# Optimization experiments

Hardware: AMD Instinct MI355X
Metric: run time of the kernel (lower is better)

## Reference

```python
import jax, jax.numpy as jnp
import numpy as np

EMBED = 1024
HEADS = 16
HEAD_DIM = EMBED // HEADS


def setup_inputs() -> dict:
    key = jax.random.key(0)
    ks = jax.random.split(key, 7)
    N, S = 2, 2048
    k = jax.random.normal(ks[0], (N, S, EMBED), dtype=jnp.float32)
    q = jax.random.normal(ks[1], (N, S, EMBED), dtype=jnp.float32)
    v = jax.random.normal(ks[2], (N, S, EMBED), dtype=jnp.float32)
    sc = 1.0 / np.sqrt(HEAD_DIM)
    # nn.Linear weights, applied as x @ W.T
    Wk = jax.random.normal(ks[3], (HEAD_DIM, HEAD_DIM), dtype=jnp.float32) * sc
    Wq = jax.random.normal(ks[4], (HEAD_DIM, HEAD_DIM), dtype=jnp.float32) * sc
    Wv = jax.random.normal(ks[5], (HEAD_DIM, HEAD_DIM), dtype=jnp.float32) * sc
    Wo = jax.random.normal(ks[6], (EMBED, EMBED), dtype=jnp.float32) / np.sqrt(EMBED)
    return {"k": k, "q": q, "v": v, "Wk": Wk, "Wq": Wq, "Wv": Wv, "Wo": Wo}


def reference(k, q, v, Wk, Wq, Wv, Wo):
    N, S, _ = q.shape
    # reshape to [N, S, H, D]; per-head projection weights shared across heads
    kh = jnp.einsum('nshd,ed->nshe', k.reshape(N, S, HEADS, HEAD_DIM), Wk)
    qh = jnp.einsum('nshd,ed->nshe', q.reshape(N, S, HEADS, HEAD_DIM), Wq)
    vh = jnp.einsum('nshd,ed->nshe', v.reshape(N, S, HEADS, HEAD_DIM), Wv)
    # energy: [N, H, q_len, k_len]
    energy = jnp.einsum('nqhd,nkhd->nhqk', qh, kh)
    attn = jax.nn.softmax(energy / jnp.sqrt(jnp.float32(HEAD_DIM)), axis=-1)
    out = jnp.einsum('nhqk,nkhd->nqhd', attn, vh).reshape(N, S, EMBED)
    return out @ Wo.T
```

## Files before the change

### kernel.cpp

```cpp
#include <hip/hip_runtime.h>

#define SQ   2048
#define HEADS 16
#define HD   64
#define EMB  1024

typedef __attribute__((ext_vector_type(2))) __fp16 h2;
typedef __attribute__((ext_vector_type(4))) __fp16 h4;
typedef __attribute__((ext_vector_type(8))) __fp16 h8;
typedef __attribute__((ext_vector_type(4))) float f4;
typedef unsigned short USH;
typedef unsigned int   UI;

__device__ __forceinline__ UI pkh(float a, float b) {
    h2 v = __builtin_amdgcn_cvt_pkrtz(a, b);
    return __builtin_bit_cast(UI, v);
}

__device__ __forceinline__ void glds16(const void* g, void* l) {
    __builtin_amdgcn_global_load_lds(
        (const __attribute__((address_space(1))) unsigned int*)g,
        (__attribute__((address_space(3))) unsigned int*)l, 16, 0, 0);
}

__global__ __launch_bounds__(256) void proj_fused(
    const float* __restrict__ q_in, const float* __restrict__ k_in,
    const float* __restrict__ v_in, const float* __restrict__ Wq,
    const float* __restrict__ Wk,   const float* __restrict__ Wv,
    const float* __restrict__ Wo,
    USH* __restrict__ Qh, USH* __restrict__ Kh, USH* __restrict__ Vt,
    USH* __restrict__ Wob)
{
    int t = threadIdx.x;
    if (blockIdx.y == 3) {
        int i = blockIdx.x * 256 + t;
        for (int j = 0; j < 4; ++j) {
            float4 v = ((const float4*)Wo)[i + j * 65536];
            uint2 pk; pk.x = pkh(v.x, v.y); pk.y = pkh(v.z, v.w);
            *(uint2*)(Wob + ((size_t)i + (size_t)j * 65536) * 4) = pk;
        }
        return;
    }
    const float* X = (blockIdx.y == 0) ? q_in : (blockIdx.y == 1) ? k_in : v_in;
    const float* W = (blockIdx.y == 0) ? Wq   : (blockIdx.y == 1) ? Wk   : Wv;
    float scale    = (blockIdx.y == 0) ? 0.18033688011112043f : 1.0f;

    int bx = (blockIdx.x & 7) * 32 + (blockIdx.x >> 3);

    __shared__ __align__(16) USH Xl[256][72];
    __shared__ __align__(16) USH Wl[64][72];

    const float4* Xg = (const float4*)(X + (size_t)bx * 16384);
    for (int j = 0; j < 16; ++j) {
        int f = t + j * 256;
        float4 v = Xg[f];
        int row = f >> 4; int col = (f & 15) << 2;
        uint2 pk; pk.x = pkh(v.x, v.y); pk.y = pkh(v.z, v.w);
        *(uint2*)&Xl[row][col] = pk;
    }
    const float4* Wg = (const float4*)W;
    for (int j = 0; j < 4; ++j) {
        int f = t + j * 256;
        float4 v = Wg[f];
        int row = f >> 4; int col = (f & 15) << 2;
        uint2 pk; pk.x = pkh(v.x, v.y); pk.y = pkh(v.z, v.w);
        *(uint2*)&Wl[row][col] = pk;
    }
    __syncthreads();

    int wv = t >> 6, lane = t & 63, l4 = lane & 15, quad = lane >> 4;

    h8 wf[4][2], xf[4][2];
    for (int et = 0; et < 4; ++et)
        for (int ks = 0; ks < 2; ++ks)
            wf[et][ks] = *(const h8*)&Wl[et * 16 + l4][ks * 32 + quad * 8];
    for (int rt = 0; rt < 4; ++rt)
        for (int ks = 0; ks < 2; ++ks)
            xf[rt][ks] = *(const h8*)&Xl[wv * 64 + rt * 16 + l4][ks * 32 + quad * 8];

    f4 acc[4][4];
    for (int et = 0; et < 4; ++et)
        for (int rt = 0; rt < 4; ++rt) acc[et][rt] = (f4)(0.0f);
    for (int et = 0; et < 4; ++et)
        for (int rt = 0; rt < 4; ++rt)
            for (int ks = 0; ks < 2; ++ks)
                acc[et][rt] = __builtin_amdgcn_mfma_f32_16x16x32_f16(
                    wf[et][ks], xf[rt][ks], acc[et][rt], 0, 0, 0);

    if (blockIdx.y == 2) {
        int ns0 = bx * 16 + wv * 4;
        int n = ns0 >> 11, s = ns0 & 2047;
        for (int et = 0; et < 4; ++et)
            for (int j = 0; j < 4; ++j) {
                int e = et * 16 + quad * 4 + j;
                uint2 pk;
                pk.x = pkh(acc[et][0][j], acc[et][1][j]);
                pk.y = pkh(acc[et][2][j], acc[et][3][j]);
                *(uint2*)(Vt + (((size_t)(n * HEADS + l4) * HD + e) * SQ + s)) = pk;
            }
    } else {
        USH* Out = (blockIdx.y == 0) ? Qh : Kh;
        for (int rt = 0; rt < 4; ++rt) {
            int ns = bx * 16 + wv * 4 + rt;
            int n = ns >> 11, s = ns & 2047;
            USH* ob = Out + (((size_t)(n * HEADS) + l4) * SQ + s) * HD;
            for (int et = 0; et < 4; ++et) {
                uint2 pk;
                pk.x = pkh(acc[et][rt][0] * scale, acc[et][rt][1] * scale);
                pk.y = pkh(acc[et][rt][2] * scale, acc[et][rt][3] * scale);
                *(uint2*)(ob + et * 16 + quad * 4) = pk;
            }
        }
    }
}

__device__ __forceinline__ void stage_k(const USH* __restrict__ Kg,
                                        int kt, USH* Kd, int w, int lane)
{
#pragma unroll
    for (int j = 0; j < 2; ++j) {
        int s = (w * 2 + j) * 64 + lane;
        int r = s >> 3, c = (s & 7) ^ (r & 7);
        glds16(Kg + kt * 4096 + r * 64 + c * 8, Kd + s * 8);
    }
}
__device__ __forceinline__ void stage_v(const USH* __restrict__ Vg,
                                        int kt, USH* Vd, int w, int lane)
{
#pragma unroll
    for (int j = 0; j < 2; ++j) {
        int s = (w * 2 + j) * 64 + lane;
        int r = s >> 3, c = (s & 7) ^ (r & 7);
        glds16(Vg + r * SQ + kt * 64 + c * 8, Vd + s * 8);
    }
}

__global__ __launch_bounds__(256, 3) void attn_kernel(
    const USH* __restrict__ Qh, const USH* __restrict__ Kh,
    const USH* __restrict__ Vt, USH* __restrict__ Oh)
{
    __shared__ union {
        struct { USH K[2][4096]; USH V[4][4096]; } s;
        struct { float Osum[64][68]; float Lsum[64]; } r;
    } lds;

    int t = threadIdx.x, w = t >> 6, lane = t & 63;
    int l4 = lane & 15, quad = lane >> 4;
    int b = blockIdx.x;
    int nh = b & 31;
    int q0 = (b >> 5) * 64;
    const USH* Qg = Qh + ((size_t)nh * SQ + q0) * HD;
    const USH* Kg = Kh + (size_t)nh * SQ * HD;
    const USH* Vg = Vt + (size_t)nh * HD * SQ;

    h8 bq[4][2];
#pragma unroll
    for (int qt = 0; qt < 4; ++qt)
#pragma unroll
        for (int ks = 0; ks < 2; ++ks)
            bq[qt][ks] = *(const h8*)(Qg + (size_t)(qt * 16 + l4) * HD + ks * 32 + quad * 8);

    f4 o[4][4];
#pragma unroll
    for (int dt = 0; dt < 4; ++dt)
#pragma unroll
        for (int qt = 0; qt < 4; ++qt) o[dt][qt] = (f4)(0.0f);
    float lsum[4] = {0.f, 0.f, 0.f, 0.f};

    int key = w * 16 + l4;
    int kslot0 = key * 8 + (quad ^ (key & 7));
    int kslot1 = key * 8 + ((4 + quad) ^ (key & 7));
    int dchunk = w * 2 + (quad >> 1);
    int vbyte  = (quad & 1) * 4;
    int vs[4];
#pragma unroll
    for (int dt = 0; dt < 4; ++dt) {
        int d = dt * 16 + l4;
        vs[dt] = (d * 8 + (dchunk ^ (d & 7))) * 8 + vbyte;
    }

    stage_k(Kg, 0, lds.s.K[0], w, lane);
    stage_v(Vg, 0, lds.s.V[0], w, lane);

    uint2 pA[4];
    for (int i = 0; i < 16; ++i) {
        int t0 = 2 * i, t1 = 2 * i + 1;
        USH* Vb0 = lds.s.V[t0 & 3];
        USH* Vb1 = lds.s.V[t1 & 3];

        __syncthreads();
        stage_k(Kg, t0 + 1, lds.s.K[1], w, lane);
        stage_v(Vg, t0 + 1, Vb1, w, lane);

        {
            h8 ak0 = *(const h8*)(lds.s.K[0] + kslot0 * 8);
            h8 ak1 = *(const h8*)(lds.s.K[0] + kslot1 * 8);
#pragma unroll
            for (int qt = 0; qt < 4; ++qt) {
                f4 s0 = __builtin_amdgcn_mfma_f32_16x16x32_f16(ak0, bq[qt][0], (f4)(0.0f), 0, 0, 0);
                f4 sc = __builtin_amdgcn_mfma_f32_16x16x32_f16(ak1, bq[qt][1], s0, 0, 0, 0);
                float p0 = __builtin_amdgcn_exp2f(sc[0]);
                float p1 = __builtin_amdgcn_exp2f(sc[1]);
                float p2 = __builtin_amdgcn_exp2f(sc[2]);
                float p3 = __builtin_amdgcn_exp2f(sc[3]);
                lsum[qt] += (p0 + p1) + (p2 + p3);
                pA[qt].x = pkh(p0, p1); pA[qt].y = pkh(p2, p3);
            }
        }

        __syncthreads();
        if (t1 + 1 < 32) {
            stage_k(Kg, t1 + 1, lds.s.K[0], w, lane);
            stage_v(Vg, t1 + 1, lds.s.V[(t1 + 1) & 3], w, lane);
        }

        uint2 pB[4];
        {
            h8 ak0 = *(const h8*)(lds.s.K[1] + kslot0 * 8);
            h8 ak1 = *(const h8*)(lds.s.K[1] + kslot1 * 8);
#pragma unroll
            for (int qt = 0; qt < 4; ++qt) {
                f4 s0 = __builtin_amdgcn_mfma_f32_16x16x32_f16(ak0, bq[qt][0], (f4)(0.0f), 0, 0, 0);
                f4 sc = __builtin_amdgcn_mfma_f32_16x16x32_f16(ak1, bq[qt][1], s0, 0, 0, 0);
                float p0 = __builtin_amdgcn_exp2f(sc[0]);
                float p1 = __builtin_amdgcn_exp2f(sc[1]);
                float p2 = __builtin_amdgcn_exp2f(sc[2]);
                float p3 = __builtin_amdgcn_exp2f(sc[3]);
                lsum[qt] += (p0 + p1) + (p2 + p3);
                pB[qt].x = pkh(p0, p1); pB[qt].y = pkh(p2, p3);
            }
        }

        h8 av8[4];
#pragma unroll
        for (int dt = 0; dt < 4; ++dt) {
            uint2 lo = *(const uint2*)(Vb0 + vs[dt]);
            uint2 hi = *(const uint2*)(Vb1 + vs[dt]);
            uint4 u; u.x = lo.x; u.y = lo.y; u.z = hi.x; u.w = hi.y;
            av8[dt] = __builtin_bit_cast(h8, u);
        }

#pragma unroll
        for (int dt = 0; dt < 4; ++dt)
#pragma unroll
            for (int qt = 0; qt < 4; ++qt) {
                uint4 u; u.x = pA[qt].x; u.y = pA[qt].y;
                u.z = pB[qt].x; u.w = pB[qt].y;
                h8 pp = __builtin_bit_cast(h8, u);
                o[dt][qt] = __builtin_amdgcn_mfma_f32_16x16x32_f16(
                    av8[dt], pp, o[dt][qt], 0, 0, 0);
            }
    }

#pragma unroll
    for (int qt = 0; qt < 4; ++qt) {
        lsum[qt] += __shfl_xor(lsum[qt], 16, 64);
        lsum[qt] += __shfl_xor(lsum[qt], 32, 64);
    }

    __syncthreads();
    for (int ph = 0; ph < 4; ++ph) {
        if (w == ph) {
            for (int dt = 0; dt < 4; ++dt)
                for (int qt = 0; qt < 4; ++qt) {
                    float* dst = &lds.r.Osum[qt * 16 + l4][dt * 16 + quad * 4];
                    f4 val = o[dt][qt];
                    if (ph) val += *(const f4*)dst;
                    *(f4*)dst = val;
                }
            if (quad == 0)
                for (int qt = 0; qt < 4; ++qt) {
                    int qi = qt * 16 + l4;
                    lds.r.Lsum[qi] = ph ? (lds.r.Lsum[qi] + lsum[qt]) : lsum[qt];
                }
        }
        __syncthreads();
    }

    int n = nh >> 4, h = nh & 15;
    int q = t >> 2, d0 = (t & 3) * 16;
    float inv = 1.0f / lds.r.Lsum[q];
    float vv[16];
#pragma unroll
    for (int i = 0; i < 4; ++i) {
        f4 x = *(const f4*)&lds.r.Osum[q][d0 + i * 4];
        vv[i * 4 + 0] = x[0] * inv; vv[i * 4 + 1] = x[1] * inv;
        vv[i * 4 + 2] = x[2] * inv; vv[i * 4 + 3] = x[3] * inv;
    }
    uint4 ou0, ou1;
    ou0.x = pkh(vv[0], vv[1]);   ou0.y = pkh(vv[2], vv[3]);
    ou0.z = pkh(vv[4], vv[5]);   ou0.w = pkh(vv[6], vv[7]);
    ou1.x = pkh(vv[8], vv[9]);   ou1.y = pkh(vv[10], vv[11]);
    ou1.z = pkh(vv[12], vv[13]); ou1.w = pkh(vv[14], vv[15]);
    USH* ob = Oh + ((size_t)(n * SQ + q0 + q)) * EMB + h * HD + d0;
    *(uint4*)ob = ou0;
    *(uint4*)(ob + 8) = ou1;
}

__global__ __launch_bounds__(256, 4) void gemm_bt(const USH* __restrict__ A,
                                                  const USH* __restrict__ B,
                                                  float* __restrict__ C)
{
    __shared__ __align__(16) USH Al[2][4096];
    __shared__ __align__(16) USH Bl[2][4096];
    int t = threadIdx.x, w = t >> 6, lane = t & 63;
    int l4 = lane & 15, quad = lane >> 4;
    int b = blockIdx.x;
    int m0 = (b & 63) * 64;
    int n0 = (b >> 6) * 64;
    int wm = (w >> 1) * 32, wn = (w & 1) * 32;

    f4 acc[2][2];
    for (int mt = 0; mt < 2; ++mt)
        for (int nt = 0; nt < 2; ++nt) acc[mt][nt] = (f4)(0.0f);

    int aslot[2][2], bslot[2][2];
#pragma unroll
    for (int mt = 0; mt < 2; ++mt)
#pragma unroll
        for (int ks = 0; ks < 2; ++ks) {
            int m = wm + mt * 16 + l4;
            aslot[mt][ks] = m * 8 + ((ks * 4 + quad) ^ (m & 7));
            int nn = wn + mt * 16 + l4;
            bslot[mt][ks] = nn * 8 + ((ks * 4 + quad) ^ (nn & 7));
        }

#pragma unroll
    for (int j = 0; j < 2; ++j) {
        int s = (w * 2 + j) * 64 + lane;
        int r = s >> 3, c = (s & 7) ^ (r & 7);
        glds16(A + (size_t)(m0 + r) * 1024 + c * 8, Al[0] + s * 8);
        glds16(B + (size_t)(n0 + r) * 1024 + c * 8, Bl[0] + s * 8);
    }

    for (int ki = 0; ki < 16; ++ki) {
        int cur = ki & 1;
        __syncthreads();
        if (ki + 1 < 16) {
            int k0 = (ki + 1) * 64;
#pragma unroll
            for (int j = 0; j < 2; ++j) {
                int s = (w * 2 + j) * 64 + lane;
                int r = s >> 3, c = (s & 7) ^ (r & 7);
                glds16(A + (size_t)(m0 + r) * 1024 + k0 + c * 8, Al[cur ^ 1] + s * 8);
                glds16(B + (size_t)(n0 + r) * 1024 + k0 + c * 8, Bl[cur ^ 1] + s * 8);
            }
        }

        h8 a[2][2], bf[2][2];
#pragma unroll
        for (int mt = 0; mt < 2; ++mt)
#pragma unroll
            for (int ks = 0; ks < 2; ++ks) {
                a[mt][ks]  = *(const h8*)(Al[cur] + aslot[mt][ks] * 8);
                bf[mt][ks] = *(const h8*)(Bl[cur] + bslot[mt][ks] * 8);
            }
#pragma unroll
        for (int mt = 0; mt < 2; ++mt)
#pragma unroll
            for (int nt = 0; nt < 2; ++nt)
#pragma unroll
                for (int ks = 0; ks < 2; ++ks)
                    acc[mt][nt] = __builtin_amdgcn_mfma_f32_16x16x32_f16(
                        a[mt][ks], bf[nt][ks], acc[mt][nt], 0, 0, 0);
    }

    for (int mt = 0; mt < 2; ++mt)
        for (int nt = 0; nt < 2; ++nt)
            for (int r = 0; r < 4; ++r)
                C[(size_t)(m0 + wm + mt * 16 + quad * 4 + r) * 1024 +
                  (n0 + wn + nt * 16 + l4)] = acc[mt][nt][r];
}

extern "C" void kernel_launch(void* const* d_in, const int* in_sizes, int n_in,
                              void* d_out, int out_size, void* d_ws, size_t ws_size,
                              hipStream_t stream) {
    const float* k_in = (const float*)d_in[0];
    const float* q_in = (const float*)d_in[1];
    const float* v_in = (const float*)d_in[2];
    const float* Wk   = (const float*)d_in[3];
    const float* Wq   = (const float*)d_in[4];
    const float* Wv   = (const float*)d_in[5];
    const float* Wo   = (const float*)d_in[6];
    float* out = (float*)d_out;

    char* ws = (char*)d_ws;
    USH* Qh  = (USH*)(ws);
    USH* Kh  = (USH*)(ws + 8388608);
    USH* Vt  = (USH*)(ws + 16777216);
    USH* Oh  = (USH*)(ws + 25165824);
    USH* Wob = (USH*)(ws + 33554432);

    proj_fused<<<dim3(256, 4), dim3(256), 0, stream>>>(
        q_in, k_in, v_in, Wq, Wk, Wv, Wo, Qh, Kh, Vt, Wob);
    attn_kernel<<<dim3(1024), dim3(256), 0, stream>>>(Qh, Kh, Vt, Oh);
    gemm_bt<<<dim3(1024), dim3(256), 0, stream>>>(Oh, Wob, out);
}
```

Before: 187.0 us.

## Process 128 queries per attention block with two key-split wave pairs

```diff
diff --git a/kernel.cpp b/kernel.cpp
--- a/kernel.cpp
+++ b/kernel.cpp
@@ -140,15 +140,16 @@
     const USH* __restrict__ Vt, USH* __restrict__ Oh)
 {
     __shared__ union {
-        struct { USH K[2][4096]; USH V[4][4096]; } s;
-        struct { float Osum[64][68]; float Lsum[64]; } r;
+        struct { USH K[2][4096]; USH V[2][4096]; } s;
+        struct { float Osum[128][68]; float Lsum[128]; } r;
     } lds;
 
     int t = threadIdx.x, w = t >> 6, lane = t & 63;
     int l4 = lane & 15, quad = lane >> 4;
+    int qg = w >> 1, ws = w & 1;
     int b = blockIdx.x;
     int nh = b & 31;
-    int q0 = (b >> 5) * 64;
+    int q0 = (b >> 5) * 128;
     const USH* Qg = Qh + ((size_t)nh * SQ + q0) * HD;
     const USH* Kg = Kh + (size_t)nh * SQ * HD;
     const USH* Vg = Vt + (size_t)nh * HD * SQ;
@@ -158,7 +159,8 @@
     for (int qt = 0; qt < 4; ++qt)
 #pragma unroll
         for (int ks = 0; ks < 2; ++ks)
-            bq[qt][ks] = *(const h8*)(Qg + (size_t)(qt * 16 + l4) * HD + ks * 32 + quad * 8);
+            bq[qt][ks] = *(const h8*)(Qg + (size_t)(qg * 64 + qt * 16 + l4) * HD +
+                                      ks * 32 + quad * 8);
 
     f4 o[4][4];
 #pragma unroll
@@ -167,89 +169,77 @@
         for (int qt = 0; qt < 4; ++qt) o[dt][qt] = (f4)(0.0f);
     float lsum[4] = {0.f, 0.f, 0.f, 0.f};
 
-    int key = w * 16 + l4;
-    int kslot0 = key * 8 + (quad ^ (key & 7));
-    int kslot1 = key * 8 + ((4 + quad) ^ (key & 7));
-    int dchunk = w * 2 + (quad >> 1);
-    int vbyte  = (quad & 1) * 4;
-    int vs[4];
-#pragma unroll
-    for (int dt = 0; dt < 4; ++dt) {
-        int d = dt * 16 + l4;
-        vs[dt] = (d * 8 + (dchunk ^ (d & 7))) * 8 + vbyte;
-    }
+    int kslot[2][2];
+#pragma unroll
+    for (int ksub = 0; ksub < 2; ++ksub)
+#pragma unroll
+        for (int ks = 0; ks < 2; ++ks) {
+            int key = ws * 32 + ksub * 16 + l4;
+            kslot[ksub][ks] = key * 8 + ((ks * 4 + quad) ^ (key & 7));
+        }
+    int vs[4][2];
+#pragma unroll
+    for (int dt = 0; dt < 4; ++dt)
+#pragma unroll
+        for (int ksub = 0; ksub < 2; ++ksub) {
+            int d = dt * 16 + l4;
+            int ch = ws * 4 + ksub * 2 + (quad >> 1);
+            vs[dt][ksub] = (d * 8 + (ch ^ (d & 7))) * 8 + (quad & 1) * 4;
+        }
 
     stage_k(Kg, 0, lds.s.K[0], w, lane);
     stage_v(Vg, 0, lds.s.V[0], w, lane);
 
-    uint2 pA[4];
-    for (int i = 0; i < 16; ++i) {
-        int t0 = 2 * i, t1 = 2 * i + 1;
-        USH* Vb0 = lds.s.V[t0 & 3];
-        USH* Vb1 = lds.s.V[t1 & 3];
-
+    for (int kt = 0; kt < SQ / 64; ++kt) {
+        int cur = kt & 1;
         __syncthreads();
-        stage_k(Kg, t0 + 1, lds.s.K[1], w, lane);
-        stage_v(Vg, t0 + 1, Vb1, w, lane);
-
-        {
-            h8 ak0 = *(const h8*)(lds.s.K[0] + kslot0 * 8);
-            h8 ak1 = *(const h8*)(lds.s.K[0] + kslot1 * 8);
-#pragma unroll
-            for (int qt = 0; qt < 4; ++qt) {
-                f4 s0 = __builtin_amdgcn_mfma_f32_16x16x32_f16(ak0, bq[qt][0], (f4)(0.0f), 0, 0, 0);
-                f4 sc = __builtin_amdgcn_mfma_f32_16x16x32_f16(ak1, bq[qt][1], s0, 0, 0, 0);
-                float p0 = __builtin_amdgcn_exp2f(sc[0]);
-                float p1 = __builtin_amdgcn_exp2f(sc[1]);
-                float p2 = __builtin_amdgcn_exp2f(sc[2]);
-                float p3 = __builtin_amdgcn_exp2f(sc[3]);
-                lsum[qt] += (p0 + p1) + (p2 + p3);
-                pA[qt].x = pkh(p0, p1); pA[qt].y = pkh(p2, p3);
-            }
-        }
-
-        __syncthreads();
-        if (t1 + 1 < 32) {
-            stage_k(Kg, t1 + 1, lds.s.K[0], w, lane);
-            stage_v(Vg, t1 + 1, lds.s.V[(t1 + 1) & 3], w, lane);
-        }
-
-        uint2 pB[4];
-        {
-            h8 ak0 = *(const h8*)(lds.s.K[1] + kslot0 * 8);
-            h8 ak1 = *(const h8*)(lds.s.K[1] + kslot1 * 8);
-#pragma unroll
-            for (int qt = 0; qt < 4; ++qt) {
-                f4 s0 = __builtin_amdgcn_mfma_f32_16x16x32_f16(ak0, bq[qt][0], (f4)(0.0f), 0, 0, 0);
-                f4 sc = __builtin_amdgcn_mfma_f32_16x16x32_f16(ak1, bq[qt][1], s0, 0, 0, 0);
-                float p0 = __builtin_amdgcn_exp2f(sc[0]);
-                float p1 = __builtin_amdgcn_exp2f(sc[1]);
-                float p2 = __builtin_amdgcn_exp2f(sc[2]);
-                float p3 = __builtin_amdgcn_exp2f(sc[3]);
-                lsum[qt] += (p0 + p1) + (p2 + p3);
-                pB[qt].x = pkh(p0, p1); pB[qt].y = pkh(p2, p3);
-            }
-        }
+        if (kt + 1 < SQ / 64) {
+            stage_k(Kg, kt + 1, lds.s.K[cur ^ 1], w, lane);
+            stage_v(Vg, kt + 1, lds.s.V[cur ^ 1], w, lane);
+        }
+
+        h8 ak[2][2];
+#pragma unroll
+        for (int ksub = 0; ksub < 2; ++ksub)
+#pragma unroll
+            for (int ks = 0; ks < 2; ++ks)
+                ak[ksub][ks] = *(const h8*)(lds.s.K[cur] + kslot[ksub][ks] * 8);
 
         h8 av8[4];
 #pragma unroll
         for (int dt = 0; dt < 4; ++dt) {
-            uint2 lo = *(const uint2*)(Vb0 + vs[dt]);
-            uint2 hi = *(const uint2*)(Vb1 + vs[dt]);
+            uint2 lo = *(const uint2*)(lds.s.V[cur] + vs[dt][0]);
+            uint2 hi = *(const uint2*)(lds.s.V[cur] + vs[dt][1]);
             uint4 u; u.x = lo.x; u.y = lo.y; u.z = hi.x; u.w = hi.y;
             av8[dt] = __builtin_bit_cast(h8, u);
         }
 
 #pragma unroll
-        for (int dt = 0; dt < 4; ++dt)
-#pragma unroll
-            for (int qt = 0; qt < 4; ++qt) {
-                uint4 u; u.x = pA[qt].x; u.y = pA[qt].y;
-                u.z = pB[qt].x; u.w = pB[qt].y;
-                h8 pp = __builtin_bit_cast(h8, u);
+        for (int qt = 0; qt < 4; ++qt) {
+            f4 sa = __builtin_amdgcn_mfma_f32_16x16x32_f16(ak[0][0], bq[qt][0], (f4)(0.0f), 0, 0, 0);
+            sa     = __builtin_amdgcn_mfma_f32_16x16x32_f16(ak[0][1], bq[qt][1], sa, 0, 0, 0);
+            f4 sb = __builtin_amdgcn_mfma_f32_16x16x32_f16(ak[1][0], bq[qt][0], (f4)(0.0f), 0, 0, 0);
+            sb     = __builtin_amdgcn_mfma_f32_16x16x32_f16(ak[1][1], bq[qt][1], sb, 0, 0, 0);
+
+            float a0 = __builtin_amdgcn_exp2f(sa[0]);
+            float a1 = __builtin_amdgcn_exp2f(sa[1]);
+            float a2 = __builtin_amdgcn_exp2f(sa[2]);
+            float a3 = __builtin_amdgcn_exp2f(sa[3]);
+            float b0 = __builtin_amdgcn_exp2f(sb[0]);
+            float b1 = __builtin_amdgcn_exp2f(sb[1]);
+            float b2 = __builtin_amdgcn_exp2f(sb[2]);
+            float b3 = __builtin_amdgcn_exp2f(sb[3]);
+            lsum[qt] += ((a0 + a1) + (a2 + a3)) + ((b0 + b1) + (b2 + b3));
+            uint4 u;
+            u.x = pkh(a0, a1); u.y = pkh(a2, a3);
+            u.z = pkh(b0, b1); u.w = pkh(b2, b3);
+            h8 pp = __builtin_bit_cast(h8, u);
+
+#pragma unroll
+            for (int dt = 0; dt < 4; ++dt)
                 o[dt][qt] = __builtin_amdgcn_mfma_f32_16x16x32_f16(
                     av8[dt], pp, o[dt][qt], 0, 0, 0);
-            }
+        }
     }
 
 #pragma unroll
@@ -259,18 +249,18 @@
     }
 
     __syncthreads();
-    for (int ph = 0; ph < 4; ++ph) {
-        if (w == ph) {
+    for (int ph = 0; ph < 2; ++ph) {
+        if (ws == ph) {
             for (int dt = 0; dt < 4; ++dt)
                 for (int qt = 0; qt < 4; ++qt) {
-                    float* dst = &lds.r.Osum[qt * 16 + l4][dt * 16 + quad * 4];
+                    float* dst = &lds.r.Osum[qg * 64 + qt * 16 + l4][dt * 16 + quad * 4];
                     f4 val = o[dt][qt];
                     if (ph) val += *(const f4*)dst;
                     *(f4*)dst = val;
                 }
             if (quad == 0)
                 for (int qt = 0; qt < 4; ++qt) {
-                    int qi = qt * 16 + l4;
+                    int qi = qg * 64 + qt * 16 + l4;
                     lds.r.Lsum[qi] = ph ? (lds.r.Lsum[qi] + lsum[qt]) : lsum[qt];
                 }
         }
@@ -278,23 +268,20 @@
     }
 
     int n = nh >> 4, h = nh & 15;
-    int q = t >> 2, d0 = (t & 3) * 16;
+    int q = t >> 1, dh = (t & 1) * 32;
     float inv = 1.0f / lds.r.Lsum[q];
-    float vv[16];
-#pragma unroll
-    for (int i = 0; i < 4; ++i) {
-        f4 x = *(const f4*)&lds.r.Osum[q][d0 + i * 4];
-        vv[i * 4 + 0] = x[0] * inv; vv[i * 4 + 1] = x[1] * inv;
-        vv[i * 4 + 2] = x[2] * inv; vv[i * 4 + 3] = x[3] * inv;
-    }
-    uint4 ou0, ou1;
-    ou0.x = pkh(vv[0], vv[1]);   ou0.y = pkh(vv[2], vv[3]);
-    ou0.z = pkh(vv[4], vv[5]);   ou0.w = pkh(vv[6], vv[7]);
-    ou1.x = pkh(vv[8], vv[9]);   ou1.y = pkh(vv[10], vv[11]);
-    ou1.z = pkh(vv[12], vv[13]); ou1.w = pkh(vv[14], vv[15]);
-    USH* ob = Oh + ((size_t)(n * SQ + q0 + q)) * EMB + h * HD + d0;
-    *(uint4*)ob = ou0;
-    *(uint4*)(ob + 8) = ou1;
+    UI opk[16];
+#pragma unroll
+    for (int i = 0; i < 8; ++i) {
+        f4 x = *(const f4*)&lds.r.Osum[q][dh + i * 4];
+        opk[i * 2]     = pkh(x[0] * inv, x[1] * inv);
+        opk[i * 2 + 1] = pkh(x[2] * inv, x[3] * inv);
+    }
+    USH* ob = Oh + ((size_t)(n * SQ + q0 + q)) * EMB + h * HD + dh;
+    *(uint4*)(ob)      = *(uint4*)&opk[0];
+    *(uint4*)(ob + 8)  = *(uint4*)&opk[4];
+    *(uint4*)(ob + 16) = *(uint4*)&opk[8];
+    *(uint4*)(ob + 24) = *(uint4*)&opk[12];
 }
 
 __global__ __launch_bounds__(256, 4) void gemm_bt(const USH* __restrict__ A,
@@ -393,6 +380,6 @@
 
     proj_fused<<<dim3(256, 4), dim3(256), 0, stream>>>(
         q_in, k_in, v_in, Wq, Wk, Wv, Wo, Qh, Kh, Vt, Wob);
-    attn_kernel<<<dim3(1024), dim3(256), 0, stream>>>(Qh, Kh, Vt, Oh);
+    attn_kernel<<<dim3(512), dim3(256), 0, stream>>>(Qh, Kh, Vt, Oh);
     gemm_bt<<<dim3(1024), dim3(256), 0, stream>>>(Oh, Wob, out);
 }
```

Measured after the change: 195.4 us. 1.05x slower.
